# Performance work log

Measured on AMD Instinct MI355X. Metric: run time of the kernel, lower is better.

Reference implementation:

```python
import jax, jax.numpy as jnp
import numpy as np

B, S, D = 2, 2048, 1024   # batch, seq, hidden_dim
I = 512                   # intermediate_dim (per-expert FFN width)
E = 16                    # num_experts
TOP_K = 2


def setup_inputs() -> dict:
    key = jax.random.key(0)
    ks = jax.random.split(key, 10)
    sc_d = 1.0 / np.sqrt(D)
    sc_i = 1.0 / np.sqrt(I)
    return {
        "x": jax.random.normal(ks[0], (B, S, D), dtype=jnp.float32),
        # router gate: Linear(D -> E) with bias (nnx.Linear default)
        "gate_w": jax.random.normal(ks[1], (D, E), dtype=jnp.float32) * sc_d,
        "gate_b": jnp.zeros((E,), dtype=jnp.float32),
        # shared expert MLP (SwiGLU: down(silu(gate(x)) * up(x)))
        "shared_wg": jax.random.normal(ks[2], (D, I), dtype=jnp.float32) * sc_d,
        "shared_wu": jax.random.normal(ks[3], (D, I), dtype=jnp.float32) * sc_d,
        "shared_wd": jax.random.normal(ks[4], (I, D), dtype=jnp.float32) * sc_i,
        # routed experts, stacked on leading E axis
        "experts_wg": jax.random.normal(ks[5], (E, D, I), dtype=jnp.float32) * sc_d,
        "experts_wu": jax.random.normal(ks[6], (E, D, I), dtype=jnp.float32) * sc_d,
        "experts_wd": jax.random.normal(ks[7], (E, I, D), dtype=jnp.float32) * sc_i,
    }


def _mlp(x, wg, wu, wd):
    # SwiGLU MLP: down(silu(gate(x)) * up(x))
    return jnp.einsum("bsi,id->bsd", jax.nn.silu(x @ wg) * (x @ wu), wd)


def reference(x, gate_w, gate_b, shared_wg, shared_wu, shared_wd,
              experts_wg, experts_wu, experts_wd):
    # router: sigmoid logits -> top_k -> normalize by sum of selected scores
    router_logits = jax.nn.sigmoid(x @ gate_w + gate_b)          # [B,S,E]
    expert_values, expert_indices = jax.lax.top_k(router_logits, k=TOP_K)
    expert_values = expert_values / jnp.sum(expert_values, axis=-1, keepdims=True)

    # dense all-expert compute (faithful to source): [B,S,E,D]
    hg = jnp.einsum("bsd,edi->bsei", x, experts_wg)
    hu = jnp.einsum("bsd,edi->bsei", x, experts_wu)
    all_outputs = jnp.einsum("bsei,eid->bsed", jax.nn.silu(hg) * hu, experts_wd)

    # gather top-k expert outputs: [B,S,K,D]
    selected = jnp.take_along_axis(all_outputs, expert_indices[..., None], axis=2)
    expert_weighted = jnp.sum(expert_values[..., None] * selected, axis=2)  # [B,S,D]

    return x + _mlp(x, shared_wg, shared_wu, shared_wd) + expert_weighted
```

## Files before the change

### kernel.cpp

```cpp
#include <hip/hip_runtime.h>
#include <stdint.h>

typedef __attribute__((ext_vector_type(8))) short short8;
typedef __attribute__((ext_vector_type(4))) float f32x4;

#define TOKENS 4096
#define DDIM 1024
#define IDIM 512
#define NEXP 16
#define NEXP1 17
#define CSTRIDE 32
#define MAXMB 112

#define OFF_WGU   0ull
#define OFF_WD    35651584ull
#define OFF_XB    53477376ull
#define OFF_HGU   61865984ull
#define OFF_H     87031808ull
#define OFF_TOK   99614720ull
#define OFF_REC   99893248ull
#define OFF_WREC  99926016ull
#define OFF_CNT   100171776ull
#define OFF_BASE  100175872ull

__device__ __forceinline__ float bf2f(unsigned short u) {
    union { uint32_t i; float f; } v; v.i = ((uint32_t)u) << 16; return v.f;
}
__device__ __forceinline__ unsigned short f2bf(float f) {
    union { float f; uint32_t i; } v; v.f = f;
    uint32_t r = v.i + 0x7FFFu + ((v.i >> 16) & 1u);
    return (unsigned short)(r >> 16);
}
__device__ __forceinline__ void cp16(const unsigned short* g, unsigned short* l) {
    __builtin_amdgcn_global_load_lds(
        (const __attribute__((address_space(1))) uint32_t*)g,
        (__attribute__((address_space(3))) uint32_t*)l, 16, 0, 0);
}

__global__ __launch_bounds__(256)
void k_transpose(const float* __restrict__ eg, const float* __restrict__ eu,
                 const float* __restrict__ ed, const float* __restrict__ sg,
                 const float* __restrict__ su, const float* __restrict__ sd,
                 unsigned short* __restrict__ Wgu, unsigned short* __restrict__ Wd)
{
    int z = blockIdx.z;
    int e = z / 3, m = z % 3;
    int R = (m == 2) ? 512 : 1024;
    int C = (m == 2) ? 1024 : 512;
    int r0 = blockIdx.y * 64, c0 = blockIdx.x * 64;
    if (r0 >= R || c0 >= C) return;
    const float* src;
    if (m == 0)      src = (e < 16) ? eg + (size_t)e * 524288 : sg;
    else if (m == 1) src = (e < 16) ? eu + (size_t)e * 524288 : su;
    else             src = (e < 16) ? ed + (size_t)e * 524288 : sd;

    __shared__ float tl[64 * 65];
    const int tid = threadIdx.x;

    {
        const int lr = tid >> 4;
        const int lc = (tid & 15) * 4;
        #pragma unroll
        for (int ps = 0; ps < 4; ++ps) {
            int r = ps * 16 + lr;
            float4 v = *(const float4*)(src + (size_t)(r0 + r) * C + (c0 + lc));
            float* d = &tl[r * 65 + lc];
            d[0] = v.x; d[1] = v.y; d[2] = v.z; d[3] = v.w;
        }
    }
    __syncthreads();

    {
        const int w = tid >> 6, l = tid & 63;
        const int kb = (l & 7) * 8;
        #pragma unroll
        for (int p = 0; p < 2; ++p) {
            int nl = p * 32 + w * 8 + (l >> 3);
            unsigned short ov[8];
            #pragma unroll
            for (int j = 0; j < 8; ++j)
                ov[j] = f2bf(tl[(kb + j) * 65 + nl]);
            int n = c0 + nl;
            int k = r0 + kb;
            unsigned short* dst;
            if (m < 2) dst = Wgu + (size_t)e * 1048576 + (size_t)(2 * n + m) * 1024 + k;
            else       dst = Wd  + (size_t)e * 524288  + (size_t)n * 512 + k;
            *(uint4*)dst = *(uint4*)ov;
        }
    }
}

__global__ void k_xconv(const float* __restrict__ x, unsigned short* __restrict__ xb,
                        int* __restrict__ tok)
{
    int i = blockIdx.x * 256 + threadIdx.x;
    float4 v = ((const float4*)x)[i];
    ushort4 b;
    b.x = f2bf(v.x); b.y = f2bf(v.y); b.z = f2bf(v.z); b.w = f2bf(v.w);
    ((ushort4*)xb)[i] = b;
    if (i < TOKENS) tok[16 * 4096 + i] = i;
}

__global__ __launch_bounds__(512, 4)
void k_router(const float* __restrict__ x, const float* __restrict__ gw,
              const float* __restrict__ gb, int* __restrict__ tok,
              int2* __restrict__ rec, float2* __restrict__ wrec,
              int* __restrict__ counts)
{
    __shared__ float gws[1024 * 12];

    const int t = blockIdx.x * 8 + (threadIdx.x >> 6);
    const int lane = threadIdx.x & 63;
    const float* xr = x + (size_t)t * DDIM;

    float xv[16];
    #pragma unroll
    for (int kk = 0; kk < 16; ++kk) xv[kk] = xr[kk * 64 + lane];

    float v[16];

    for (int p = 0; p < 2; ++p) {
        __syncthreads();
        #pragma unroll
        for (int c = 0; c < 4; ++c) {
            int idx = threadIdx.x + c * 512;
            int k = idx >> 1;
            int h = (idx & 1) * 4;
            float4 g4 = *(const float4*)(gw + k * 16 + p * 8 + h);
            *(float4*)&gws[k * 12 + h] = g4;
        }
        __syncthreads();

        double a[8];
        #pragma unroll
        for (int j = 0; j < 8; ++j) a[j] = 0.0;

        #pragma unroll
        for (int kk = 0; kk < 16; ++kk) {
            int kl = kk * 64 + lane;
            float4 gA = *(const float4*)&gws[kl * 12];
            float4 gB = *(const float4*)&gws[kl * 12 + 4];
            double xd = (double)xv[kk];
            a[0] += xd * (double)gA.x; a[1] += xd * (double)gA.y;
            a[2] += xd * (double)gA.z; a[3] += xd * (double)gA.w;
            a[4] += xd * (double)gB.x; a[5] += xd * (double)gB.y;
            a[6] += xd * (double)gB.z; a[7] += xd * (double)gB.w;
        }

        #pragma unroll
        for (int off = 32; off > 0; off >>= 1) {
            #pragma unroll
            for (int j = 0; j < 8; ++j)
                a[j] += __shfl_xor(a[j], off, 64);
        }

        #pragma unroll
        for (int j = 0; j < 8; ++j)
            v[p * 8 + j] = 1.0f / (1.0f + expf(-(float)(a[j] + (double)gb[p * 8 + j])));
    }

    if (lane == 0) {
        int i0 = 0;
        #pragma unroll
        for (int e = 1; e < 16; ++e) if (v[e] > v[i0]) i0 = e;
        int i1 = (i0 == 0) ? 1 : 0;
        #pragma unroll
        for (int e = 0; e < 16; ++e) if (e != i0 && e != i1 && v[e] > v[i1]) i1 = e;
        float s = v[i0] + v[i1];
        float w0 = v[i0] / s, w1 = v[i1] / s;
        int p0 = atomicAdd(&counts[i0 * CSTRIDE], 1);
        tok[i0 * 4096 + p0] = t;
        int p1 = atomicAdd(&counts[i1 * CSTRIDE], 1);
        tok[i1 * 4096 + p1] = t;
        rec[t]  = make_int2(i0 * 4096 + p0, i1 * 4096 + p1);
        wrec[t] = make_float2(w0, w1);
    }
}

__global__ void k_prefix(int* counts, int* bases, int* mbp)
{
    if (threadIdx.x == 0 && blockIdx.x == 0) {
        counts[16 * CSTRIDE] = TOKENS;
        int a = 0, b = 0;
        for (int e = 0; e < NEXP1; ++e) {
            int c = counts[e * CSTRIDE];
            bases[e] = a; a += c;
            mbp[e] = b;  b += (c + 127) >> 7;
        }
        bases[17] = a;
        mbp[17] = b;
        bases[18] = a; bases[19] = a;
        mbp[18] = b;   mbp[19] = b;
    }
}


#define WAITV8 asm volatile("s_waitcnt vmcnt(8)" ::: "memory")
#define WAITV0 asm volatile("s_waitcnt vmcnt(0)" ::: "memory")
#define BAR    __builtin_amdgcn_s_barrier()

#define STAGE8(BUF, KK) do {                                                  \
    cp16(ag0 + (KK),      &As[BUF][0][wb]);                                   \
    cp16(ag0 + (KK) + 32, &As[BUF][1][wb]);                                   \
    cp16(ag1 + (KK),      &As[BUF][0][wb + 512]);                             \
    cp16(ag1 + (KK) + 32, &As[BUF][1][wb + 512]);                             \
    cp16(bg0 + (KK),      &Bs[BUF][0][wb]);                                   \
    cp16(bg0 + (KK) + 32, &Bs[BUF][1][wb]);                                   \
    cp16(bg1 + (KK),      &Bs[BUF][0][wb + 512]);                             \
    cp16(bg1 + (KK) + 32, &Bs[BUF][1][wb + 512]);                             \
} while (0)

#define CSTEP(BUF) do {                                                       \
    short8 va0[4], va1[4], vb0[4], vb1[4];                                    \
    _Pragma("unroll")                                                         \
    for (int i = 0; i < 4; ++i) {                                             \
        va0[i] = *(const short8*)&As[BUF][0][(wm*64 + i*16 + mc)*32 + qs];    \
        va1[i] = *(const short8*)&As[BUF][1][(wm*64 + i*16 + mc)*32 + qs];    \
    }                                                                         \
    _Pragma("unroll")                                                         \
    for (int j = 0; j < 4; ++j) {                                             \
        vb0[j] = *(const short8*)&Bs[BUF][0][(wn*64 + j*16 + mc)*32 + qs];    \
        vb1[j] = *(const short8*)&Bs[BUF][1][(wn*64 + j*16 + mc)*32 + qs];    \
    }                                                                         \
    _Pragma("unroll")                                                         \
    for (int i = 0; i < 4; ++i)                                               \
        _Pragma("unroll")                                                     \
        for (int j = 0; j < 4; ++j)                                           \
            acc[i][j] = __builtin_amdgcn_mfma_f32_16x16x32_bf16(va0[i], vb0[j], acc[i][j], 0, 0, 0); \
    _Pragma("unroll")                                                         \
    for (int i = 0; i < 4; ++i)                                               \
        _Pragma("unroll")                                                     \
        for (int j = 0; j < 4; ++j)                                           \
            acc[i][j] = __builtin_amdgcn_mfma_f32_16x16x32_bf16(va1[i], vb1[j], acc[i][j], 0, 0, 0); \
} while (0)

template <int MODE>
__global__ __launch_bounds__(256, 2)
void k_gemm(const unsigned short* __restrict__ Amat, const unsigned short* __restrict__ Bmat,
            const int* __restrict__ tok, const int* __restrict__ counts,
            const int* __restrict__ bases, const int* __restrict__ mbp,
            unsigned short* __restrict__ Out)
{
    constexpr int K = (MODE == 0) ? 1024 : 512;
    const int my = blockIdx.y;

    int bb[20], mm[20];
    {
        const int4* b4 = (const int4*)bases;
        const int4* m4 = (const int4*)mbp;
        #pragma unroll
        for (int i = 0; i < 5; ++i) {
            *(int4*)&bb[i * 4] = b4[i];
            *(int4*)&mm[i * 4] = m4[i];
        }
    }
    if (my >= mm[17]) return;
    int e = 0, me = mm[0], ba = bb[0], bn = bb[1];
    #pragma unroll
    for (int i = 1; i <= 16; ++i)
        if (my >= mm[i]) { e = i; me = mm[i]; ba = bb[i]; bn = bb[i + 1]; }
    const int cnt  = bn - ba;
    const int m0   = (my - me) * 128;
    const int base = ba;
    const int n0   = blockIdx.x * 128;

    __shared__ unsigned short As[2][2][128 * 32];
    __shared__ unsigned short Bs[2][2][128 * 32];

    const int tid  = threadIdx.x;
    const int wave = tid >> 6;
    const int lane = tid & 63;
    const int lrow = lane >> 2;
    const int lseg = (lane & 3) ^ ((lrow >> 1) & 3);

    const int wb = wave * 1024;

    int ar0 = m0 + wave * 32 + lrow;      if (ar0 > cnt - 1) ar0 = cnt - 1;
    int ar1 = m0 + wave * 32 + 16 + lrow; if (ar1 > cnt - 1) ar1 = cnt - 1;
    size_t ai0, ai1;
    if (MODE == 0) { ai0 = (size_t)tok[e * 4096 + ar0]; ai1 = (size_t)tok[e * 4096 + ar1]; }
    else           { ai0 = (size_t)(base + ar0);        ai1 = (size_t)(base + ar1); }
    const unsigned short* ag0 = Amat + ai0 * K + lseg * 8;
    const unsigned short* ag1 = Amat + ai1 * K + lseg * 8;
    const size_t eoff = (size_t)e * 1024 * K;
    const unsigned short* bg0 = Bmat + eoff + (size_t)(n0 + wave * 32 + lrow) * K + lseg * 8;
    const unsigned short* bg1 = Bmat + eoff + (size_t)(n0 + wave * 32 + 16 + lrow) * K + lseg * 8;

    const int wm = wave & 1, wn = wave >> 1;
    const int q = lane >> 4, mc = lane & 15;
    const int qs = (q ^ ((mc >> 1) & 3)) * 8;

    f32x4 acc[4][4];
    #pragma unroll
    for (int i = 0; i < 4; ++i)
        #pragma unroll
        for (int j = 0; j < 4; ++j) acc[i][j] = (f32x4){0.f, 0.f, 0.f, 0.f};

    STAGE8(0, 0);

    for (int k0 = 0; k0 < K; k0 += 128) {
        STAGE8(1, k0 + 64);
        WAITV8;
        BAR;
        CSTEP(0);
        BAR;
        if (k0 + 128 < K) { STAGE8(0, k0 + 128); WAITV8; }
        else              { WAITV0; }
        BAR;
        CSTEP(1);
        BAR;
    }

    #pragma unroll
    for (int i = 0; i < 4; ++i) {
        int lr = wm * 64 + i * 16 + q * 4;
        #pragma unroll
        for (int r = 0; r < 4; ++r) {
            int mrow = m0 + lr + r;
            if (mrow >= cnt) continue;
            #pragma unroll
            for (int j = 0; j < 4; ++j) {
                int gc = n0 + wn * 64 + j * 16 + mc;
                float val = acc[i][j][r];
                if (MODE == 0) {
                    float other = __shfl_xor(val, 1, 64);
                    float g = (mc & 1) ? other : val;
                    float u = (mc & 1) ? val : other;
                    float h = g / (1.0f + __expf(-g)) * u;
                    if ((mc & 1) == 0)
                        Out[(size_t)(base + mrow) * 512 + (gc >> 1)] = f2bf(h);
                } else {
                    Out[(size_t)(base + mrow) * 1024 + gc] = f2bf(val);
                }
            }
        }
    }
}

__global__ void k_combine(const float* __restrict__ x, const unsigned short* __restrict__ Hs,
                          const int2* __restrict__ rec, const float2* __restrict__ wrec,
                          const int* __restrict__ bases, float* __restrict__ out)
{
    int t = blockIdx.x * 2 + (threadIdx.x >> 7);
    int c = (threadIdx.x & 127) * 8;
    int2 r = rec[t];
    float2 w = wrec[t];
    int s0 = bases[r.x >> 12] + (r.x & 4095);
    int s1 = bases[r.y >> 12] + (r.y & 4095);
    int ss = 8192 + t;

    unsigned short h0[8], h1[8], hs[8];
    *(uint4*)h0 = *(const uint4*)(Hs + (size_t)s0 * 1024 + c);
    *(uint4*)h1 = *(const uint4*)(Hs + (size_t)s1 * 1024 + c);
    *(uint4*)hs = *(const uint4*)(Hs + (size_t)ss * 1024 + c);
    const float* xr = x + (size_t)t * 1024 + c;
    float o[8];
    #pragma unroll
    for (int j = 0; j < 8; ++j)
        o[j] = xr[j] + bf2f(hs[j]) + w.x * bf2f(h0[j]) + w.y * bf2f(h1[j]);
    float* orow = out + (size_t)t * 1024 + c;
    *(float4*)orow       = *(float4*)&o[0];
    *(float4*)(orow + 4) = *(float4*)&o[4];
}

extern "C" void kernel_launch(void* const* d_in, const int* in_sizes, int n_in,
                              void* d_out, int out_size, void* d_ws, size_t ws_size,
                              hipStream_t stream)
{
    const float* x  = (const float*)d_in[0];
    const float* gw = (const float*)d_in[1];
    const float* gb = (const float*)d_in[2];
    const float* sg = (const float*)d_in[3];
    const float* su = (const float*)d_in[4];
    const float* sd = (const float*)d_in[5];
    const float* eg = (const float*)d_in[6];
    const float* eu = (const float*)d_in[7];
    const float* ed = (const float*)d_in[8];
    float* out = (float*)d_out;
    char* ws = (char*)d_ws;

    unsigned short* Wgu = (unsigned short*)(ws + OFF_WGU);
    unsigned short* Wd  = (unsigned short*)(ws + OFF_WD);
    unsigned short* xb  = (unsigned short*)(ws + OFF_XB);
    unsigned short* Hgu = (unsigned short*)(ws + OFF_HGU);
    unsigned short* H   = (unsigned short*)(ws + OFF_H);
    int*    tok   = (int*)(ws + OFF_TOK);
    int2*   rec   = (int2*)(ws + OFF_REC);
    float2* wrec  = (float2*)(ws + OFF_WREC);
    int*    counts= (int*)(ws + OFF_CNT);
    int*    bases = (int*)(ws + OFF_BASE);
    int*    mbp   = bases + 20;

    (void)hipMemsetAsync(counts, 0, 4096, stream);
    k_transpose<<<dim3(16, 16, 51), 256, 0, stream>>>(eg, eu, ed, sg, su, sd, Wgu, Wd);
    k_xconv<<<4096, 256, 0, stream>>>(x, xb, tok);
    k_router<<<512, 512, 0, stream>>>(x, gw, gb, tok, rec, wrec, counts);
    k_prefix<<<1, 64, 0, stream>>>(counts, bases, mbp);
    k_gemm<0><<<dim3(8, MAXMB), 256, 0, stream>>>(xb, Wgu, tok, counts, bases, mbp, H);
    k_gemm<1><<<dim3(8, MAXMB), 256, 0, stream>>>(H, Wd, tok, counts, bases, mbp, Hgu);
    k_combine<<<2048, 256, 0, stream>>>(x, Hgu, rec, wrec, bases, out);
}
```

Before: 284.4 us.

## Enlarge grouped GEMM tiles to 256x256 with 8 waves and triple-buffered pipeline

The grouped expert GEMMs move from 128x128 tiles with 4 waves to 256x256 tiles with 8 waves (512 threads). Each wave now computes a 128x64 sub-tile. The K loop becomes a triple-buffered, 32-wide pipeline that interleaves global-to-LDS copies with the MFMA phases and raises wave priority around the MFMAs. The aim is more data reuse per loaded byte and better overlap of loads with compute. In exchange, expert padding to 256 rows wastes more work, there are fewer blocks to fill the CUs, and register pressure rises with 128 accumulators per lane.

```diff
diff --git a/kernel.cpp b/kernel.cpp
--- a/kernel.cpp
+++ b/kernel.cpp
@@ -10,7 +10,7 @@
 #define NEXP 16
 #define NEXP1 17
 #define CSTRIDE 32
-#define MAXMB 112
+#define MAXMB 64
 
 #define OFF_WGU   0ull
 #define OFF_WD    35651584ull
@@ -185,7 +185,7 @@
         for (int e = 0; e < NEXP1; ++e) {
             int c = counts[e * CSTRIDE];
             bases[e] = a; a += c;
-            mbp[e] = b;  b += (c + 127) >> 7;
+            mbp[e] = b;  b += (c + 255) >> 8;
         }
         bases[17] = a;
         mbp[17] = b;
@@ -195,53 +195,23 @@
 }
 
 
-#define WAITV8 asm volatile("s_waitcnt vmcnt(8)" ::: "memory")
-#define WAITV0 asm volatile("s_waitcnt vmcnt(0)" ::: "memory")
-#define BAR    __builtin_amdgcn_s_barrier()
-
-#define STAGE8(BUF, KK) do {                                                  \
-    cp16(ag0 + (KK),      &As[BUF][0][wb]);                                   \
-    cp16(ag0 + (KK) + 32, &As[BUF][1][wb]);                                   \
-    cp16(ag1 + (KK),      &As[BUF][0][wb + 512]);                             \
-    cp16(ag1 + (KK) + 32, &As[BUF][1][wb + 512]);                             \
-    cp16(bg0 + (KK),      &Bs[BUF][0][wb]);                                   \
-    cp16(bg0 + (KK) + 32, &Bs[BUF][1][wb]);                                   \
-    cp16(bg1 + (KK),      &Bs[BUF][0][wb + 512]);                             \
-    cp16(bg1 + (KK) + 32, &Bs[BUF][1][wb + 512]);                             \
+#define STAGE4(TT, BUF) do {                                                  \
+    const int kq = (TT) * 32;                                                 \
+    cp16(ag0 + kq, AsW + (BUF) * 8192);                                       \
+    cp16(ag1 + kq, AsW + (BUF) * 8192 + 4096);                                \
+    cp16(bg0 + kq, BsW + (BUF) * 8192);                                       \
+    cp16(bg1 + kq, BsW + (BUF) * 8192 + 4096);                                \
 } while (0)
 
-#define CSTEP(BUF) do {                                                       \
-    short8 va0[4], va1[4], vb0[4], vb1[4];                                    \
-    _Pragma("unroll")                                                         \
-    for (int i = 0; i < 4; ++i) {                                             \
-        va0[i] = *(const short8*)&As[BUF][0][(wm*64 + i*16 + mc)*32 + qs];    \
-        va1[i] = *(const short8*)&As[BUF][1][(wm*64 + i*16 + mc)*32 + qs];    \
-    }                                                                         \
-    _Pragma("unroll")                                                         \
-    for (int j = 0; j < 4; ++j) {                                             \
-        vb0[j] = *(const short8*)&Bs[BUF][0][(wn*64 + j*16 + mc)*32 + qs];    \
-        vb1[j] = *(const short8*)&Bs[BUF][1][(wn*64 + j*16 + mc)*32 + qs];    \
-    }                                                                         \
-    _Pragma("unroll")                                                         \
-    for (int i = 0; i < 4; ++i)                                               \
-        _Pragma("unroll")                                                     \
-        for (int j = 0; j < 4; ++j)                                           \
-            acc[i][j] = __builtin_amdgcn_mfma_f32_16x16x32_bf16(va0[i], vb0[j], acc[i][j], 0, 0, 0); \
-    _Pragma("unroll")                                                         \
-    for (int i = 0; i < 4; ++i)                                               \
-        _Pragma("unroll")                                                     \
-        for (int j = 0; j < 4; ++j)                                           \
-            acc[i][j] = __builtin_amdgcn_mfma_f32_16x16x32_bf16(va1[i], vb1[j], acc[i][j], 0, 0, 0); \
-} while (0)
-
 template <int MODE>
-__global__ __launch_bounds__(256, 2)
+__global__ __launch_bounds__(512, 2)
 void k_gemm(const unsigned short* __restrict__ Amat, const unsigned short* __restrict__ Bmat,
             const int* __restrict__ tok, const int* __restrict__ counts,
             const int* __restrict__ bases, const int* __restrict__ mbp,
             unsigned short* __restrict__ Out)
 {
-    constexpr int K = (MODE == 0) ? 1024 : 512;
+    constexpr int K  = (MODE == 0) ? 1024 : 512;
+    constexpr int NT = K / 32;
     const int my = blockIdx.y;
 
     int bb[20], mm[20];
@@ -260,60 +230,102 @@
     for (int i = 1; i <= 16; ++i)
         if (my >= mm[i]) { e = i; me = mm[i]; ba = bb[i]; bn = bb[i + 1]; }
     const int cnt  = bn - ba;
-    const int m0   = (my - me) * 128;
+    const int m0   = (my - me) * 256;
     const int base = ba;
-    const int n0   = blockIdx.x * 128;
-
-    __shared__ unsigned short As[2][2][128 * 32];
-    __shared__ unsigned short Bs[2][2][128 * 32];
+    const int n0   = blockIdx.x * 256;
+
+    __shared__ unsigned short As[3 * 8192];
+    __shared__ unsigned short Bs[3 * 8192];
 
     const int tid  = threadIdx.x;
     const int wave = tid >> 6;
     const int lane = tid & 63;
     const int lrow = lane >> 2;
-    const int lseg = (lane & 3) ^ ((lrow >> 1) & 3);
-
-    const int wb = wave * 1024;
-
-    int ar0 = m0 + wave * 32 + lrow;      if (ar0 > cnt - 1) ar0 = cnt - 1;
-    int ar1 = m0 + wave * 32 + 16 + lrow; if (ar1 > cnt - 1) ar1 = cnt - 1;
+    const int segg = (lane & 3) ^ ((lrow >> 1) & 3);
+
+    unsigned short* AsW = As + wave * 512;
+    unsigned short* BsW = Bs + wave * 512;
+
+    int ar0 = m0 + wave * 16 + lrow;        if (ar0 > cnt - 1) ar0 = cnt - 1;
+    int ar1 = m0 + 128 + wave * 16 + lrow;  if (ar1 > cnt - 1) ar1 = cnt - 1;
     size_t ai0, ai1;
     if (MODE == 0) { ai0 = (size_t)tok[e * 4096 + ar0]; ai1 = (size_t)tok[e * 4096 + ar1]; }
     else           { ai0 = (size_t)(base + ar0);        ai1 = (size_t)(base + ar1); }
-    const unsigned short* ag0 = Amat + ai0 * K + lseg * 8;
-    const unsigned short* ag1 = Amat + ai1 * K + lseg * 8;
+    const unsigned short* ag0 = Amat + ai0 * K + segg * 8;
+    const unsigned short* ag1 = Amat + ai1 * K + segg * 8;
     const size_t eoff = (size_t)e * 1024 * K;
-    const unsigned short* bg0 = Bmat + eoff + (size_t)(n0 + wave * 32 + lrow) * K + lseg * 8;
-    const unsigned short* bg1 = Bmat + eoff + (size_t)(n0 + wave * 32 + 16 + lrow) * K + lseg * 8;
-
-    const int wm = wave & 1, wn = wave >> 1;
+    const unsigned short* bg0 = Bmat + eoff + (size_t)(n0 + wave * 16 + lrow) * K + segg * 8;
+    const unsigned short* bg1 = Bmat + eoff + (size_t)(n0 + 128 + wave * 16 + lrow) * K + segg * 8;
+
+    const int wm = wave >> 2, wn = wave & 3;
     const int q = lane >> 4, mc = lane & 15;
     const int qs = (q ^ ((mc >> 1) & 3)) * 8;
 
-    f32x4 acc[4][4];
+    f32x4 acc[8][4];
     #pragma unroll
-    for (int i = 0; i < 4; ++i)
+    for (int i = 0; i < 8; ++i)
         #pragma unroll
         for (int j = 0; j < 4; ++j) acc[i][j] = (f32x4){0.f, 0.f, 0.f, 0.f};
 
-    STAGE8(0, 0);
-
-    for (int k0 = 0; k0 < K; k0 += 128) {
-        STAGE8(1, k0 + 64);
-        WAITV8;
-        BAR;
-        CSTEP(0);
-        BAR;
-        if (k0 + 128 < K) { STAGE8(0, k0 + 128); WAITV8; }
-        else              { WAITV0; }
-        BAR;
-        CSTEP(1);
-        BAR;
+    STAGE4(0, 0);
+    STAGE4(1, 1);
+
+    int bR = 0, bS = 2;
+    for (int T = 0; T < NT; ++T) {
+        if (T + 1 < NT) { asm volatile("s_waitcnt vmcnt(4)" ::: "memory"); }
+        else            { asm volatile("s_waitcnt vmcnt(0)" ::: "memory"); }
+        __builtin_amdgcn_s_barrier();
+
+        const unsigned short* aT = As + bR * 8192;
+        const unsigned short* bT = Bs + bR * 8192;
+        const int kk = (T + 2) * 32;
+        const bool st = (T + 2 < NT);
+
+        if (st) {
+            cp16(ag0 + kk, AsW + bS * 8192);
+            cp16(ag1 + kk, AsW + bS * 8192 + 4096);
+        }
+        __builtin_amdgcn_sched_barrier(0);
+        short8 bf[4], af[4];
+        #pragma unroll
+        for (int nf = 0; nf < 4; ++nf)
+            bf[nf] = *(const short8*)&bT[(wn * 64 + nf * 16 + mc) * 32 + qs];
+        #pragma unroll
+        for (int mf = 0; mf < 4; ++mf)
+            af[mf] = *(const short8*)&aT[(wm * 128 + mf * 16 + mc) * 32 + qs];
+        __builtin_amdgcn_s_setprio(1);
+        #pragma unroll
+        for (int mf = 0; mf < 4; ++mf)
+            #pragma unroll
+            for (int nf = 0; nf < 4; ++nf)
+                acc[mf][nf] = __builtin_amdgcn_mfma_f32_16x16x32_bf16(af[mf], bf[nf], acc[mf][nf], 0, 0, 0);
+        __builtin_amdgcn_s_setprio(0);
+        __builtin_amdgcn_s_barrier();
+
+        if (st) {
+            cp16(bg0 + kk, BsW + bS * 8192);
+            cp16(bg1 + kk, BsW + bS * 8192 + 4096);
+        }
+        __builtin_amdgcn_sched_barrier(0);
+        short8 ah[4];
+        #pragma unroll
+        for (int mf = 0; mf < 4; ++mf)
+            ah[mf] = *(const short8*)&aT[(wm * 128 + (mf + 4) * 16 + mc) * 32 + qs];
+        __builtin_amdgcn_s_setprio(1);
+        #pragma unroll
+        for (int mf = 0; mf < 4; ++mf)
+            #pragma unroll
+            for (int nf = 0; nf < 4; ++nf)
+                acc[mf + 4][nf] = __builtin_amdgcn_mfma_f32_16x16x32_bf16(ah[mf], bf[nf], acc[mf + 4][nf], 0, 0, 0);
+        __builtin_amdgcn_s_setprio(0);
+
+        bR = (bR == 2) ? 0 : bR + 1;
+        bS = (bS == 2) ? 0 : bS + 1;
     }
 
     #pragma unroll
-    for (int i = 0; i < 4; ++i) {
-        int lr = wm * 64 + i * 16 + q * 4;
+    for (int i = 0; i < 8; ++i) {
+        int lr = wm * 128 + i * 16 + q * 4;
         #pragma unroll
         for (int r = 0; r < 4; ++r) {
             int mrow = m0 + lr + r;
@@ -396,7 +408,7 @@
     k_xconv<<<4096, 256, 0, stream>>>(x, xb, tok);
     k_router<<<512, 512, 0, stream>>>(x, gw, gb, tok, rec, wrec, counts);
     k_prefix<<<1, 64, 0, stream>>>(counts, bases, mbp);
-    k_gemm<0><<<dim3(8, MAXMB), 256, 0, stream>>>(xb, Wgu, tok, counts, bases, mbp, H);
-    k_gemm<1><<<dim3(8, MAXMB), 256, 0, stream>>>(H, Wd, tok, counts, bases, mbp, Hgu);
+    k_gemm<0><<<dim3(4, MAXMB), 512, 0, stream>>>(xb, Wgu, tok, counts, bases, mbp, H);
+    k_gemm<1><<<dim3(4, MAXMB), 512, 0, stream>>>(H, Wd, tok, counts, bases, mbp, Hgu);
     k_combine<<<2048, 256, 0, stream>>>(x, Hgu, rec, wrec, bases, out);
 }
```

After: 293.6 us. 3.2% more time.
